# Kernel optimization log

Measured on AMD Instinct MI355X. Metric: run time of the kernel, lower is better.

The kernel has to match this reference:

```python
import jax, jax.numpy as jnp
import numpy as np

PAD = 0
SIGMA_C = 2.0
EPS = 1e-6
LOG_SQRT_2PI = 0.9189385332046727  # log(sqrt(2*pi))

B, T_CHAR, VOCAB, D_EMB = 32, 256, 100, 384


def setup_inputs() -> dict:
    rng = np.random.default_rng(0)
    # text tokens in [1, VOCAB): avoid pad (=0) inside the utterance
    text = rng.integers(1, VOCAB, size=(B, T_CHAR), dtype=np.int64)
    # per-char durations in frames, 1..8
    durs = rng.integers(1, 9, size=(B, T_CHAR), dtype=np.int32)
    # total_time = length of repeat_interleave(text, durs) padded to batch max
    total_time = int(durs.sum(axis=-1).max())
    key = jax.random.key(0)
    embed = jax.random.normal(key, (VOCAB, D_EMB), dtype=jnp.float32)
    return {
        "text": jnp.asarray(text),
        "durs": jnp.asarray(durs),
        "embed": embed,
        "total_time": total_time,
    }


def reference(text, durs, embed, total_time):
    # Pad 2 trailing positions: pad token, zero duration (as in the original)
    text = jnp.pad(text, ((0, 0), (0, 2)), constant_values=PAD)      # [B, Tc]
    durs = jnp.pad(durs, ((0, 0), (0, 2)), constant_values=0)        # [B, Tc]
    durs_f = durs.astype(jnp.float32)

    # Gaussian centers: mid-point of each char's frame span
    csum = jnp.cumsum(durs_f, axis=-1)
    c = durs_f / 2.0 + jnp.pad(csum[:, :-1], ((0, 0), (1, 0)))       # [B, Tc]
    sig = durs_f / SIGMA_C + EPS                                     # [B, Tc]

    t = jnp.arange(total_time, dtype=jnp.float32) + 0.5              # [Tt]

    # Gaussian pdf evaluated at frame times: w[b, t, c]
    z = (t[None, :, None] - c[:, None, :]) / sig[:, None, :]         # [B, Tt, Tc]
    w = jnp.exp(-0.5 * z * z - jnp.log(sig)[:, None, :] - LOG_SQRT_2PI)

    # zero padded-char columns, normalize over chars
    char_pad = (text == PAD)[:, None, :]                             # [B, 1, Tc]
    w = jnp.where(char_pad, 0.0, w)
    w = w / (jnp.sum(w, axis=-1, keepdims=True) + EPS)

    # time positions past each utterance's total duration are padding:
    # zero the whole row, then put weight 1.0 on the last (pad) char column
    total_dur = jnp.sum(durs, axis=-1)                               # [B]
    time_pad = jnp.arange(total_time)[None, :] >= total_dur[:, None] # [B, Tt]
    w = jnp.where(time_pad[:, :, None], 0.0, w)
    w = w.at[:, :, -1].set(jnp.where(time_pad, 1.0, w[:, :, -1]))

    # aggregate gathered embeddings: [B, Tt, Tc] x [B, Tc, D] -> [B, Tt, D]
    u = jnp.einsum("btc,bcd->btd", w, embed[text])
    return u
```

## Files before the change

kernel.cpp:

```cpp
#include <hip/hip_runtime.h>

#define TC 256
#define DEMB 384
#define VOC 100
#define WIN 96
#define TTILE 32
#define WPS 104
#define CST 288
#define LOG_SQRT_2PI 0.9189385332046727f

typedef short v8s __attribute__((ext_vector_type(8)));
typedef float v4f __attribute__((ext_vector_type(4)));

__device__ __forceinline__ unsigned short f32_to_bf16_rne(float f) {
    union { float f; unsigned int u; } x; x.f = f;
    unsigned int u = x.u;
    return (unsigned short)((u + 0x7FFFu + ((u >> 16) & 1u)) >> 16);
}

__global__ __launch_bounds__(256) void prep_kernel(
    const int* __restrict__ text, const int* __restrict__ durs,
    const float* __restrict__ embed,
    unsigned short* __restrict__ ET,
    float* __restrict__ ctrA, float* __restrict__ isgA, float* __restrict__ lgA,
    int* __restrict__ j0A, int* __restrict__ totA)
{
    if (blockIdx.x < 576) {
        int i = blockIdx.x * 256 + threadIdx.x;
        int c = i % CST;
        int r = i / CST;
        int nseg = r & 15;
        int b = r >> 4;
        if (c >= TC) return;
        int v = text[b * TC + c];
        const float* erow = embed + (size_t)v * DEMB + nseg * 24;
        unsigned short* dst = ET + ((size_t)b * DEMB + nseg * 24) * CST + c;
#pragma unroll
        for (int k = 0; k < 6; ++k) {
            float4 e = *(const float4*)(erow + 4 * k);
            dst[(4 * k + 0) * CST] = f32_to_bf16_rne(e.x);
            dst[(4 * k + 1) * CST] = f32_to_bf16_rne(e.y);
            dst[(4 * k + 2) * CST] = f32_to_bf16_rne(e.z);
            dst[(4 * k + 3) * CST] = f32_to_bf16_rne(e.w);
        }
    } else {
        const int b = blockIdx.x - 576;
        const int c = threadIdx.x;
        const int lane = c & 63, wv = c >> 6;
        int d = durs[b * TC + c];
        int x = d;
#pragma unroll
        for (int ofs = 1; ofs < 64; ofs <<= 1) {
            int n = __shfl_up(x, ofs, 64);
            if (lane >= ofs) x += n;
        }
        __shared__ int s_wsum[4];
        if (lane == 63) s_wsum[wv] = x;
        __syncthreads();
        int pre = 0;
        for (int k = 0; k < wv; ++k) pre += s_wsum[k];
        int en = pre + x;
        int st = en - d;
        if (c == TC - 1) totA[b] = en;

        float df  = (float)d;
        float sig = df * 0.5f + 1e-6f;
        ctrA[b * TC + c] = (float)st + df * 0.5f;
        isgA[b * TC + c] = 1.0f / sig;
        lgA[b * TC + c]  = -logf(sig) - LOG_SQRT_2PI;

        for (int t0 = ((st + 31) >> 5) << 5; t0 < en; t0 += 32)
            j0A[b * 64 + (t0 >> 5)] = c;
    }
}

__global__ __launch_bounds__(256, 2) void gauss_embed_mfma_kernel(
    const float* __restrict__ embed,
    const unsigned short* __restrict__ ET,
    const float* __restrict__ ctrA, const float* __restrict__ isgA,
    const float* __restrict__ lgA,
    const int* __restrict__ j0A, const int* __restrict__ totA,
    float* __restrict__ out, int Tt)
{
    const int b   = blockIdx.y;
    const int t0  = blockIdx.x * TTILE;
    const int tid = threadIdx.x;
    const int totdur = totA[b];

    if (t0 >= totdur) {
        const float4* e0 = (const float4*)embed;
        int row = tid >> 3, q4 = tid & 7;
        int t = t0 + row;
        if (t < Tt) {
            float4* orow = (float4*)(out + (size_t)(b * Tt + t) * DEMB);
#pragma unroll
            for (int k = 0; k < 12; ++k) orow[q4 + 8 * k] = e0[q4 + 8 * k];
        }
        return;
    }

    const int wv   = tid >> 6;
    const int lane = tid & 63;
    const int nq   = lane & 15;
    const int q    = lane >> 4;

    __shared__ float s_ctr[WIN], s_isg[WIN], s_A[WIN];
    __shared__ __align__(16) unsigned short s_wp[TTILE * WPS];
    __shared__ float s_part[256];
    __shared__ float s_invS[TTILE];

    int j0 = j0A[b * 64 + (t0 >> 5)];
    int base = j0 - 31;
    base = base < 0 ? 0 : base;
    base &= ~7;
    if (base > TC - WIN) base = TC - WIN;

    if (tid < WIN) {
        s_ctr[tid] = ctrA[b * TC + base + tid];
        s_isg[tid] = isgA[b * TC + base + tid];
        s_A[tid]   = lgA[b * TC + base + tid];
    }
    __syncthreads();

    {
        const int t = tid & 31;
        const int g = tid >> 5;
        const float tf = (float)(t0 + t) + 0.5f;
        float lsum = 0.0f;
#pragma unroll
        for (int cc = 0; cc < 12; ++cc) {
            int c = g * 12 + cc;
            float z = (tf - s_ctr[c]) * s_isg[c];
            float w = __expf(fmaf(-0.5f * z, z, s_A[c]));
            lsum += w;
            s_wp[t * WPS + c] = f32_to_bf16_rne(w);
        }
        s_part[tid] = lsum;
    }
    __syncthreads();

    if (tid < TTILE) {
        float s = 1e-6f;
#pragma unroll
        for (int g = 0; g < 8; ++g) s += s_part[g * 32 + tid];
        s_invS[tid] = 1.0f / s;
    }
    __syncthreads();

    const unsigned short* ETb = ET + (size_t)b * DEMB * CST + base;

    v4f acc[6][2];
#pragma unroll
    for (int nt = 0; nt < 6; ++nt)
#pragma unroll
        for (int mt = 0; mt < 2; ++mt) {
            v4f z = {0.0f, 0.0f, 0.0f, 0.0f};
            acc[nt][mt] = z;
        }

#pragma unroll
    for (int ks = 0; ks < 3; ++ks) {
        const int c0 = ks * 32 + q * 8;
        v8s a0 = *(const v8s*)(s_wp + nq * WPS + c0);
        v8s a1 = *(const v8s*)(s_wp + (16 + nq) * WPS + c0);
#pragma unroll
        for (int nt = 0; nt < 6; ++nt) {
            v8s bf = *(const v8s*)(ETb + (size_t)(wv * 96 + nt * 16 + nq) * CST + c0);
            acc[nt][0] = __builtin_amdgcn_mfma_f32_16x16x32_bf16(a0, bf, acc[nt][0], 0, 0, 0);
            acc[nt][1] = __builtin_amdgcn_mfma_f32_16x16x32_bf16(a1, bf, acc[nt][1], 0, 0, 0);
        }
    }

    const bool anypad = (t0 + TTILE > totdur);
    float pe[6];
    if (anypad) {
#pragma unroll
        for (int nt = 0; nt < 6; ++nt) pe[nt] = embed[wv * 96 + nt * 16 + nq];
    }

#pragma unroll
    for (int mt = 0; mt < 2; ++mt) {
#pragma unroll
        for (int r = 0; r < 4; ++r) {
            int tl = mt * 16 + q * 4 + r;
            int t = t0 + tl;
            if (t >= Tt) continue;
            float sv = s_invS[tl];
            bool pad = anypad && (t >= totdur);
            float* orow = out + (size_t)(b * Tt + t) * DEMB + wv * 96 + nq;
#pragma unroll
            for (int nt = 0; nt < 6; ++nt) {
                float val = pad ? pe[nt] : acc[nt][mt][r] * sv;
                orow[nt * 16] = val;
            }
        }
    }
}

extern "C" void kernel_launch(void* const* d_in, const int* in_sizes, int n_in,
                              void* d_out, int out_size, void* d_ws, size_t ws_size,
                              hipStream_t stream) {
    const int*   text  = (const int*)d_in[0];
    const int*   durs  = (const int*)d_in[1];
    const float* embed = (const float*)d_in[2];
    float* out = (float*)d_out;

    const int B = 32;
    const int Tt = out_size / (B * DEMB);

    char* ws = (char*)d_ws;
    unsigned short* ET = (unsigned short*)ws;
    float* ctrA = (float*)(ws + 7077888);
    float* isgA = (float*)(ws + 7077888 + 32768);
    float* lgA  = (float*)(ws + 7077888 + 65536);
    int*   j0A  = (int*)  (ws + 7077888 + 98304);
    int*   totA = (int*)  (ws + 7077888 + 106496);

    prep_kernel<<<608, 256, 0, stream>>>(text, durs, embed, ET,
                                         ctrA, isgA, lgA, j0A, totA);

    dim3 grid((Tt + TTILE - 1) / TTILE, B);
    gauss_embed_mfma_kernel<<<grid, 256, 0, stream>>>(embed, ET, ctrA, isgA, lgA,
                                                      j0A, totA, out, Tt);
}
```

Baseline: 100.5 us.

## Scatter Gaussian weights into vocab bins and multiply by shared embedding table

The weights are no longer multiplied against a per-batch gathered, transposed embedding. Each block now accumulates the Gaussian weights per vocabulary id in shared memory with atomics, then runs the MFMA matmul against a single transposed bf16 embedding table padded to 128. This removes the large per-batch embedding gather and transpose from prep and shrinks global reads in the main kernel. In exchange it adds LDS atomic contention, a zero-fill pass and a conversion pass over the 32x136 buffer, and a fourth K-step.

```diff
diff --git a/kernel.cpp b/kernel.cpp
--- a/kernel.cpp
+++ b/kernel.cpp
@@ -3,10 +3,10 @@
 #define TC 256
 #define DEMB 384
 #define VOC 100
+#define VK 128
+#define MST 136
 #define WIN 96
 #define TTILE 32
-#define WPS 104
-#define CST 288
 #define LOG_SQRT_2PI 0.9189385332046727f
 
 typedef short v8s __attribute__((ext_vector_type(8)));
@@ -21,30 +21,18 @@
 __global__ __launch_bounds__(256) void prep_kernel(
     const int* __restrict__ text, const int* __restrict__ durs,
     const float* __restrict__ embed,
-    unsigned short* __restrict__ ET,
+    unsigned short* __restrict__ EBT,
     float* __restrict__ ctrA, float* __restrict__ isgA, float* __restrict__ lgA,
     int* __restrict__ j0A, int* __restrict__ totA)
 {
-    if (blockIdx.x < 576) {
+    if (blockIdx.x < 192) {
         int i = blockIdx.x * 256 + threadIdx.x;
-        int c = i % CST;
-        int r = i / CST;
-        int nseg = r & 15;
-        int b = r >> 4;
-        if (c >= TC) return;
-        int v = text[b * TC + c];
-        const float* erow = embed + (size_t)v * DEMB + nseg * 24;
-        unsigned short* dst = ET + ((size_t)b * DEMB + nseg * 24) * CST + c;
-#pragma unroll
-        for (int k = 0; k < 6; ++k) {
-            float4 e = *(const float4*)(erow + 4 * k);
-            dst[(4 * k + 0) * CST] = f32_to_bf16_rne(e.x);
-            dst[(4 * k + 1) * CST] = f32_to_bf16_rne(e.y);
-            dst[(4 * k + 2) * CST] = f32_to_bf16_rne(e.z);
-            dst[(4 * k + 3) * CST] = f32_to_bf16_rne(e.w);
-        }
+        int v = i & (VK - 1);
+        int n = i >> 7;
+        float val = (v < VOC) ? embed[v * DEMB + n] : 0.0f;
+        EBT[i] = f32_to_bf16_rne(val);
     } else {
-        const int b = blockIdx.x - 576;
+        const int b = blockIdx.x - 192;
         const int c = threadIdx.x;
         const int lane = c & 63, wv = c >> 6;
         int d = durs[b * TC + c];
@@ -76,7 +64,8 @@
 
 __global__ __launch_bounds__(256, 2) void gauss_embed_mfma_kernel(
     const float* __restrict__ embed,
-    const unsigned short* __restrict__ ET,
+    const int* __restrict__ text,
+    const unsigned short* __restrict__ EBT,
     const float* __restrict__ ctrA, const float* __restrict__ isgA,
     const float* __restrict__ lgA,
     const int* __restrict__ j0A, const int* __restrict__ totA,
@@ -104,21 +93,24 @@
     const int nq   = lane & 15;
     const int q    = lane >> 4;
 
+    __shared__ float s_Mf[TTILE * MST];
+    __shared__ __align__(16) unsigned short s_M[TTILE * MST];
     __shared__ float s_ctr[WIN], s_isg[WIN], s_A[WIN];
-    __shared__ __align__(16) unsigned short s_wp[TTILE * WPS];
+    __shared__ int   s_wtx[WIN];
     __shared__ float s_part[256];
     __shared__ float s_invS[TTILE];
 
     int j0 = j0A[b * 64 + (t0 >> 5)];
     int base = j0 - 31;
     base = base < 0 ? 0 : base;
-    base &= ~7;
     if (base > TC - WIN) base = TC - WIN;
 
+    for (int i = tid; i < TTILE * MST; i += 256) s_Mf[i] = 0.0f;
     if (tid < WIN) {
         s_ctr[tid] = ctrA[b * TC + base + tid];
         s_isg[tid] = isgA[b * TC + base + tid];
         s_A[tid]   = lgA[b * TC + base + tid];
+        s_wtx[tid] = text[b * TC + base + tid];
     }
     __syncthreads();
 
@@ -133,7 +125,7 @@
             float z = (tf - s_ctr[c]) * s_isg[c];
             float w = __expf(fmaf(-0.5f * z, z, s_A[c]));
             lsum += w;
-            s_wp[t * WPS + c] = f32_to_bf16_rne(w);
+            atomicAdd(&s_Mf[t * MST + s_wtx[c]], w);
         }
         s_part[tid] = lsum;
     }
@@ -145,9 +137,11 @@
         for (int g = 0; g < 8; ++g) s += s_part[g * 32 + tid];
         s_invS[tid] = 1.0f / s;
     }
+    for (int i = tid; i < TTILE * VK; i += 256) {
+        int t = i >> 7, k = i & (VK - 1);
+        s_M[t * MST + k] = f32_to_bf16_rne(s_Mf[t * MST + k]);
+    }
     __syncthreads();
-
-    const unsigned short* ETb = ET + (size_t)b * DEMB * CST + base;
 
     v4f acc[6][2];
 #pragma unroll
@@ -159,13 +153,13 @@
         }
 
 #pragma unroll
-    for (int ks = 0; ks < 3; ++ks) {
-        const int c0 = ks * 32 + q * 8;
-        v8s a0 = *(const v8s*)(s_wp + nq * WPS + c0);
-        v8s a1 = *(const v8s*)(s_wp + (16 + nq) * WPS + c0);
+    for (int ks = 0; ks < 4; ++ks) {
+        const int k0 = ks * 32 + q * 8;
+        v8s a0 = *(const v8s*)(s_M + nq * MST + k0);
+        v8s a1 = *(const v8s*)(s_M + (16 + nq) * MST + k0);
 #pragma unroll
         for (int nt = 0; nt < 6; ++nt) {
-            v8s bf = *(const v8s*)(ETb + (size_t)(wv * 96 + nt * 16 + nq) * CST + c0);
+            v8s bf = *(const v8s*)(EBT + (wv * 96 + nt * 16 + nq) * VK + k0);
             acc[nt][0] = __builtin_amdgcn_mfma_f32_16x16x32_bf16(a0, bf, acc[nt][0], 0, 0, 0);
             acc[nt][1] = __builtin_amdgcn_mfma_f32_16x16x32_bf16(a1, bf, acc[nt][1], 0, 0, 0);
         }
@@ -209,17 +203,18 @@
     const int Tt = out_size / (B * DEMB);
 
     char* ws = (char*)d_ws;
-    unsigned short* ET = (unsigned short*)ws;
-    float* ctrA = (float*)(ws + 7077888);
-    float* isgA = (float*)(ws + 7077888 + 32768);
-    float* lgA  = (float*)(ws + 7077888 + 65536);
-    int*   j0A  = (int*)  (ws + 7077888 + 98304);
-    int*   totA = (int*)  (ws + 7077888 + 106496);
-
-    prep_kernel<<<608, 256, 0, stream>>>(text, durs, embed, ET,
+    unsigned short* EBT = (unsigned short*)ws;
+    float* ctrA = (float*)(ws + 98304);
+    float* isgA = (float*)(ws + 98304 + 32768);
+    float* lgA  = (float*)(ws + 98304 + 65536);
+    int*   j0A  = (int*)  (ws + 98304 + 98304);
+    int*   totA = (int*)  (ws + 98304 + 106496);
+
+    prep_kernel<<<224, 256, 0, stream>>>(text, durs, embed, EBT,
                                          ctrA, isgA, lgA, j0A, totA);
 
     dim3 grid((Tt + TTILE - 1) / TTILE, B);
-    gauss_embed_mfma_kernel<<<grid, 256, 0, stream>>>(embed, ET, ctrA, isgA, lgA,
+    gauss_embed_mfma_kernel<<<grid, 256, 0, stream>>>(embed, text, EBT,
+                                                      ctrA, isgA, lgA,
                                                       j0A, totA, out, Tt);
 }
```

New measurement: 110.0 us. +9.5%, slower.
